# Optimization experiments

Measured on AMD Instinct MI355X. Metric: run time of the kernel, lower is better.

## Reference

```python
import jax, jax.numpy as jnp
import numpy as np

N_FLUID, N_BOX, K_MAX, KS, NCELL = 6000, 3000, 80, 4, 64
RADIUS = np.float32(0.5 * 1.5 * 6 * 0.025)  # filter_extent / 2 = 0.1125


def _ball_to_cube(p):
    """Volume-preserving ball->cube mapping (open3d ContinuousConv convention).
    p: [..., 3] coordinates in the unit ball; returns coords in [-1,1]^3."""
    eps = 1e-12
    x, y, z = p[..., 0], p[..., 1], p[..., 2]
    sq = x * x + y * y + z * z
    norm = jnp.sqrt(sq)
    rxy2 = x * x + y * y
    # sphere -> cylinder (volume preserving)
    polar = 1.25 * z * z > rxy2
    s_pol = jnp.sqrt(3.0 * norm / (norm + jnp.abs(z) + eps))
    s_eq = norm / jnp.sqrt(rxy2 + eps)
    xc = jnp.where(polar, s_pol * x, s_eq * x)
    yc = jnp.where(polar, s_pol * y, s_eq * y)
    zc = jnp.where(polar, jnp.sign(z) * norm, 1.5 * z * s_eq)
    zero = sq < 1e-12
    xc = jnp.where(zero, 0.0, xc)
    yc = jnp.where(zero, 0.0, yc)
    zc = jnp.where(zero, 0.0, zc)
    # cylinder -> cube (area-preserving disc -> square on xy)
    rxy = jnp.sqrt(xc * xc + yc * yc)
    FP = 4.0 / np.pi
    safe_x = jnp.where(jnp.abs(xc) < eps, eps, xc)
    safe_y = jnp.where(jnp.abs(yc) < eps, eps, yc)
    cond = jnp.abs(xc) >= jnp.abs(yc)
    u1 = jnp.sign(xc) * rxy
    v1 = u1 * FP * jnp.arctan(yc / safe_x)
    v2 = jnp.sign(yc) * rxy
    u2 = v2 * FP * jnp.arctan(xc / safe_y)
    u = jnp.where(cond, u1, u2)
    v = jnp.where(cond, v1, v2)
    small = rxy < eps
    u = jnp.where(small, 0.0, u)
    v = jnp.where(small, 0.0, v)
    return jnp.stack([u, v, zc], axis=-1)


def build_neighbors(pos_in, pos_out, ignore_self):
    """Fixed-radius neighbor search (capped at K_MAX) + window + trilinear
    interpolation cells/weights. Returns idx [No,K], cells [No,K,8] int32,
    coef [No,K,8] (trilinear weight * poly6 window * validity)."""
    d = pos_in[None, :, :] - pos_out[:, None, :]            # [No,Ni,3]
    d2 = jnp.sum(d * d, axis=-1)
    if ignore_self:
        ii = jnp.arange(pos_out.shape[0])
        d2 = jnp.where(ii[:, None] == ii[None, :], jnp.inf, d2)
    neg = jnp.where(d2 <= RADIUS * RADIUS, -d2, -jnp.inf)
    vals, idx = jax.lax.top_k(neg, K_MAX)                   # [No,K]
    valid = (vals > -jnp.inf).astype(pos_in.dtype)
    rel = (pos_in[idx] - pos_out[:, None, :]) / RADIUS      # [No,K,3] unit ball
    r2 = jnp.sum(rel * rel, axis=-1)
    win = jnp.clip((1.0 - r2) ** 3, 0.0, 1.0) * valid       # poly6 window
    g = jnp.clip((_ball_to_cube(rel) + 1.0) * 0.5 * (KS - 1), 0.0, KS - 1.0)
    i0 = jnp.clip(jnp.floor(g), 0, KS - 2).astype(jnp.int32)
    t = g - i0.astype(g.dtype)
    cells, tw = [], []
    for dx in (0, 1):
        for dy in (0, 1):
            for dz in (0, 1):
                w = ((t[..., 0] if dx else 1.0 - t[..., 0])
                     * (t[..., 1] if dy else 1.0 - t[..., 1])
                     * (t[..., 2] if dz else 1.0 - t[..., 2]))
                cell = ((i0[..., 2] + dz) * KS + (i0[..., 1] + dy)) * KS + (i0[..., 0] + dx)
                cells.append(cell)
                tw.append(w)
    cells = jnp.stack(cells, axis=-1)                       # [No,K,8]
    coef = jnp.stack(tw, axis=-1) * win[..., None]          # [No,K,8]
    return idx, cells, coef


def apply_cconv(feats_in, idx, cells, coef, W, b):
    """Continuous conv: scatter neighbor feats into 64 kernel cells per query,
    then contract with the filter. W: [64, F, O]."""
    N, K = idx.shape
    F = feats_in.shape[-1]
    nf = feats_in[idx]                                      # [N,K,F]
    S = jnp.zeros((N * NCELL, F), feats_in.dtype)
    row = (jnp.arange(N, dtype=jnp.int32) * NCELL)[:, None]
    for c in range(8):                                      # 8 trilinear corners
        flat = (row + cells[..., c]).reshape(-1)
        S = S.at[flat].add((coef[..., c:c + 1] * nf).reshape(-1, F))
    return jnp.einsum('ncf,cfo->no', S.reshape(N, NCELL, F), W) + b


def setup_inputs() -> dict:
    key = jax.random.key(0)
    ks = jax.random.split(key, 16)

    def p(i, shape, scale=0.05):
        return (scale * jax.random.normal(ks[i], shape)).astype(jnp.float32)

    return {
        'pos': jax.random.uniform(ks[0], (N_FLUID, 3), dtype=jnp.float32),
        'vel': jax.random.normal(ks[1], (N_FLUID, 3), dtype=jnp.float32),
        'box': jax.random.uniform(ks[2], (N_BOX, 3), dtype=jnp.float32),
        'box_feats': jax.random.normal(ks[3], (N_BOX, 3), dtype=jnp.float32),
        'cf_w': p(4, (NCELL, 4, 32)), 'cf_b': jnp.zeros((32,), jnp.float32),
        'co_w': p(5, (NCELL, 3, 32)), 'co_b': jnp.zeros((32,), jnp.float32),
        'd0_w': p(6, (4, 32)), 'd0_b': jnp.zeros((32,), jnp.float32),
        'c1_w': p(7, (NCELL, 96, 64)), 'c1_b': jnp.zeros((64,), jnp.float32),
        'd1_w': p(8, (96, 64)), 'd1_b': jnp.zeros((64,), jnp.float32),
        'c2_w': p(9, (NCELL, 64, 64)), 'c2_b': jnp.zeros((64,), jnp.float32),
        'd2_w': p(10, (64, 64)), 'd2_b': jnp.zeros((64,), jnp.float32),
        'c3_w': p(11, (NCELL, 64, 3)), 'c3_b': jnp.zeros((3,), jnp.float32),
        'd3_w': p(12, (64, 3)), 'd3_b': jnp.zeros((3,), jnp.float32),
    }


def reference(pos, vel, box, box_feats, cf_w, cf_b, co_w, co_b, d0_w, d0_b,
              c1_w, c1_b, d1_w, d1_b, c2_w, c2_b, d2_w, d2_b, c3_w, c3_b,
              d3_w, d3_b):
    fidx, fcells, fcoef = build_neighbors(pos, pos, True)
    oidx, ocells, ocoef = build_neighbors(box, pos, False)
    ff = jnp.concatenate([jnp.ones_like(pos[:, :1]), vel], axis=-1)  # [N,4]
    a_cf = apply_cconv(ff, fidx, fcells, fcoef, cf_w, cf_b)
    a_co = apply_cconv(box_feats, oidx, ocells, ocoef, co_w, co_b)
    a_d0 = ff @ d0_w + d0_b
    x = jnp.concatenate([a_co, a_cf, a_d0], axis=-1)                 # [N,96]
    for cw, cb, dw, db in ((c1_w, c1_b, d1_w, d1_b),
                           (c2_w, c2_b, d2_w, d2_b),
                           (c3_w, c3_b, d3_w, d3_b)):
        h = jax.nn.relu(x)
        y = apply_cconv(h, fidx, fcells, fcoef, cw, cb) + (h @ dw + db)
        x = y + x if y.shape[-1] == x.shape[-1] else y
    return x * (1.0 / 128.0)  # pos_correction [N,3]
```

## Files before the change

kernel.cpp:

```cpp
#include <hip/hip_runtime.h>
#include <math.h>

namespace {

constexpr int NQ  = 6000;
constexpr int NB  = 3000;
constexpr int K   = 80;
constexpr float RAD = 0.1125f;
constexpr float R2  = RAD * RAD;
constexpr float EPSF = 1e-12f;

constexpr int GS  = 8;
constexpr int NC  = GS*GS*GS;
constexpr int NO  = 65 * 64;
constexpr int NBLK = (NQ + 3) / 4;
constexpr int NBLK8 = ((NBLK + 7) / 8) * 8;

typedef __attribute__((ext_vector_type(8))) short bf16x8;
typedef __attribute__((ext_vector_type(4))) float f32x4;

__device__ __forceinline__ float sgn(float x) {
    return (x > 0.f) ? 1.f : ((x < 0.f) ? -1.f : 0.f);
}

__device__ __forceinline__ unsigned int bf16rne(float f) {
    unsigned int u = __float_as_uint(f);
    return (u + 0x7fffu + ((u >> 16) & 1u)) >> 16;
}
__device__ __forceinline__ float bf16f(unsigned short u) {
    return __uint_as_float(((unsigned int)u) << 16);
}
__device__ __forceinline__ int cell_of(float x, float y, float z) {
    int cx = min(max((int)(x * (float)GS), 0), GS-1);
    int cy = min(max((int)(y * (float)GS), 0), GS-1);
    int cz = min(max((int)(z * (float)GS), 0), GS-1);
    return (cz*GS + cy)*GS + cx;
}

__device__ void coef_store(float ddx, float ddy, float ddz, int slot,
                           int* __restrict__ cells, float* __restrict__ coefs)
{
    float rx = ddx / RAD, ry = ddy / RAD, rz = ddz / RAD;
    float r2 = rx*rx + ry*ry + rz*rz;
    float w1 = 1.f - r2;
    float win = (w1 > 0.f) ? w1*w1*w1 : 0.f;
    float norm = sqrtf(r2);
    float rxy2 = rx*rx + ry*ry;
    float xc, yc, zc;
    if (r2 < 1e-12f) {
        xc = yc = zc = 0.f;
    } else if (1.25f * rz * rz > rxy2) {
        float s = sqrtf(3.0f * norm / (norm + fabsf(rz) + EPSF));
        xc = s * rx; yc = s * ry; zc = sgn(rz) * norm;
    } else {
        float s = norm / sqrtf(rxy2 + EPSF);
        xc = s * rx; yc = s * ry; zc = 1.5f * rz * s;
    }
    float rxy = sqrtf(xc*xc + yc*yc);
    const float FP = (float)(4.0 / M_PI);
    float u, v;
    if (rxy < EPSF) {
        u = 0.f; v = 0.f;
    } else if (fabsf(xc) >= fabsf(yc)) {
        float sx = (fabsf(xc) < EPSF) ? EPSF : xc;
        u = sgn(xc) * rxy;
        v = u * FP * atanf(yc / sx);
    } else {
        float sy = (fabsf(yc) < EPSF) ? EPSF : yc;
        v = sgn(yc) * rxy;
        u = v * FP * atanf(xc / sy);
    }
    float gx = fminf(fmaxf((u  + 1.f) * 0.5f * 3.f, 0.f), 3.f);
    float gy = fminf(fmaxf((v  + 1.f) * 0.5f * 3.f, 0.f), 3.f);
    float gz = fminf(fmaxf((zc + 1.f) * 0.5f * 3.f, 0.f), 3.f);
    int ix = min((int)floorf(gx), 2);
    int iy = min((int)floorf(gy), 2);
    int iz = min((int)floorf(gz), 2);
    float tx = gx - (float)ix, ty = gy - (float)iy, tz = gz - (float)iz;
    cells[slot] = iz*16 + iy*4 + ix;
    float wx[2] = {1.f - tx, tx}, wy[2] = {1.f - ty, ty}, wz[2] = {1.f - tz, tz};
    float* cf = coefs + (size_t)slot * 8;
#pragma unroll
    for (int c = 0; c < 8; ++c)
        cf[c] = wx[c >> 2] * wy[(c >> 1) & 1] * wz[c & 1] * win;
}

__global__ __launch_bounds__(512) void scan_kernel(
    const int* __restrict__ gcnt,
    int* __restrict__ gs_f, int* __restrict__ gs_b,
    int* __restrict__ cur_f, int* __restrict__ cur_b)
{
    __shared__ int tmp[NC];
    int tid = threadIdx.x;
#pragma unroll
    for (int a = 0; a < 2; ++a) {
        int cntv = gcnt[a*NC + tid];
        tmp[tid] = cntv;
        __syncthreads();
        for (int off = 1; off < NC; off <<= 1) {
            int v = (tid >= off) ? tmp[tid - off] : 0;
            __syncthreads();
            tmp[tid] += v;
            __syncthreads();
        }
        int* gsd = a ? gs_b : gs_f;
        int* cur = a ? cur_b : cur_f;
        int excl = tmp[tid] - cntv;
        gsd[tid] = excl;
        cur[tid] = excl;
        if (tid == NC - 1) gsd[NC] = tmp[tid];
        __syncthreads();
    }
}

__global__ __launch_bounds__(256) void scatter_pts_kernel(
    const float* __restrict__ pos, const float* __restrict__ box,
    int* __restrict__ cur_f, int* __restrict__ cur_b,
    float* __restrict__ spf, int* __restrict__ sif,
    float* __restrict__ spb, int* __restrict__ sib)
{
    int t = blockIdx.x * blockDim.x + threadIdx.x;
    if (t < NQ) {
        float x = pos[t*3], y = pos[t*3+1], z = pos[t*3+2];
        int dst = atomicAdd(&cur_f[cell_of(x,y,z)], 1);
        spf[dst*3] = x; spf[dst*3+1] = y; spf[dst*3+2] = z;
        sif[dst] = t;
    } else if (t < NQ + NB) {
        int b = t - NQ;
        float x = box[b*3], y = box[b*3+1], z = box[b*3+2];
        int dst = atomicAdd(&cur_b[cell_of(x,y,z)], 1);
        spb[dst*3] = x; spb[dst*3+1] = y; spb[dst*3+2] = z;
        sib[dst] = b;
    }
}

__global__ __launch_bounds__(256) void nn2gc_kernel(
    const float* __restrict__ pos,
    const float* __restrict__ spf, const int* __restrict__ sif, const int* __restrict__ gsf,
    const float* __restrict__ spb, const int* __restrict__ sib, const int* __restrict__ gsb,
    int* __restrict__ f_cnt, int* __restrict__ f_idx, float* __restrict__ f_d2,
    int* __restrict__ f_cell, float* __restrict__ f_coef,
    int* __restrict__ b_cnt, int* __restrict__ b_idx, float* __restrict__ b_d2,
    int* __restrict__ b_cell, float* __restrict__ b_coef)
{
    int gw = (blockIdx.x * blockDim.x + threadIdx.x) >> 6;
    int lane = threadIdx.x & 63;
    if (gw >= 2 * NQ) return;
    bool isF = gw < NQ;
    int wid = isF ? gw : gw - NQ;
    const float* sp = isF ? spf : spb;
    const int*   si = isF ? sif : sib;
    const int*   gs = isF ? gsf : gsb;
    int*   cnt   = isF ? f_cnt  : b_cnt;
    int*   idxs  = isF ? f_idx  : b_idx;
    float* d2s   = isF ? f_d2   : b_d2;
    int*   cells = isF ? f_cell : b_cell;
    float* coefs = isF ? f_coef : b_coef;
    float qx = pos[wid*3+0], qy = pos[wid*3+1], qz = pos[wid*3+2];
    int cx = min(max((int)(qx * (float)GS), 0), GS-1);
    int cy = min(max((int)(qy * (float)GS), 0), GS-1);
    int cz = min(max((int)(qz * (float)GS), 0), GS-1);
    int x0 = max(cx-1, 0), x1 = min(cx+1, GS-1);
    int base = wid * K;
    int c = 0;
    for (int dz = -1; dz <= 1; ++dz) {
        int z = cz + dz; if ((unsigned)z >= (unsigned)GS) continue;
        for (int dy = -1; dy <= 1; ++dy) {
            int y = cy + dy; if ((unsigned)y >= (unsigned)GS) continue;
            int row = (z*GS + y)*GS;
            int s0 = gs[row + x0], s1 = gs[row + x1 + 1];
            for (int j0 = s0; j0 < s1; j0 += 64) {
                int ii = j0 + lane;
                float d2 = 1e30f; int oj = 0;
                float ddx = 0.f, ddy = 0.f, ddz = 0.f;
                if (ii < s1) {
                    oj = si[ii];
                    ddx = sp[ii*3+0]-qx; ddy = sp[ii*3+1]-qy; ddz = sp[ii*3+2]-qz;
                    d2 = ddx*ddx + ddy*ddy + ddz*ddz;
                    if (isF && oj == wid) d2 = 1e30f;
                }
                bool hit = d2 <= R2;
                unsigned long long m = __ballot(hit);
                int pc = __popcll(m);
                if (pc == 0) continue;
                if (c + pc <= K) {
                    if (hit) {
                        int p = c + __popcll(m & ((1ull << lane) - 1ull));
                        idxs[base + p] = oj;
                        d2s [base + p] = d2;
                        coef_store(ddx, ddy, ddz, base + p, cells, coefs);
                    }
                    c += pc;
                } else {
                    while (m) {
                        int l = __ffsll((unsigned long long)m) - 1;
                        m &= m - 1ull;
                        float dd = __shfl(d2, l);
                        int jv = __shfl(oj, l);
                        float ax = __shfl(ddx, l), ay = __shfl(ddy, l), az = __shfl(ddz, l);
                        int slot = -1;
                        if (c < K) { slot = c; c++; }
                        else {
                            float mx = -1.f; int am = 0;
                            for (int s = 0; s < K; ++s) {
                                float v = d2s[base + s];
                                if (v > mx) { mx = v; am = s; }
                            }
                            if (dd < mx) slot = am;
                        }
                        if (slot >= 0 && lane == 0) {
                            idxs[base + slot] = jv;
                            d2s [base + slot] = dd;
                            coef_store(ax, ay, az, base + slot, cells, coefs);
                        }
                    }
                }
            }
        }
    }
    if (lane == 0) cnt[wid] = c;
}

__global__ __launch_bounds__(256) void gather0_kernel(
    const int* __restrict__ order,
    const int* __restrict__ f_cnt, const int* __restrict__ f_idx,
    const int* __restrict__ f_cell, const float* __restrict__ f_coef,
    const int* __restrict__ b_cnt, const int* __restrict__ b_idx,
    const int* __restrict__ b_cell, const float* __restrict__ b_coef,
    const unsigned short* __restrict__ G0f, const unsigned short* __restrict__ G0b,
    const float* __restrict__ cfb, const float* __restrict__ cob,
    float* __restrict__ x1)
{
    __shared__ __align__(16) float coefF[K * 8];
    __shared__ __align__(16) float coefB[K * 8];
    __shared__ int jF[K], cF[K], jB[K], cBx[K];
    __shared__ float partF[8][32], partB[8][32];
    int lb = (blockIdx.x & 7) * (gridDim.x >> 3) + (blockIdx.x >> 3);
    int tid = threadIdx.x;
    int wv = tid >> 6, lane = tid & 63;
    int h = lane >> 5, o = lane & 31;
    int r = wv * 2 + h;
    int n = order[lb];
    int cnf = f_cnt[n], cnb = b_cnt[n];
    {
        const float4* srcF = (const float4*)(f_coef + (size_t)n * K * 8);
        const float4* srcB = (const float4*)(b_coef + (size_t)n * K * 8);
        for (int i = tid; i < cnf * 2; i += 256) ((float4*)coefF)[i] = srcF[i];
        for (int i = tid; i < cnb * 2; i += 256) ((float4*)coefB)[i] = srcB[i];
        for (int i = tid; i < cnf; i += 256) { jF[i] = f_idx[n*K + i]; cF[i]  = f_cell[n*K + i]; }
        for (int i = tid; i < cnb; i += 256) { jB[i] = b_idx[n*K + i]; cBx[i] = b_cell[n*K + i]; }
    }
    __syncthreads();
    float af = 0.f;
#pragma unroll 2
    for (int k = r; k < cnf; k += 8) {
        const unsigned short* Gj = G0f + (size_t)jF[k] * 2048 + (size_t)cF[k] * 32 + o;
        float4 cA = *reinterpret_cast<const float4*>(coefF + k*8);
        float4 cB = *reinterpret_cast<const float4*>(coefF + k*8 + 4);
        af += cA.x * bf16f(Gj[ 0 * 32]);
        af += cA.y * bf16f(Gj[16 * 32]);
        af += cA.z * bf16f(Gj[ 4 * 32]);
        af += cA.w * bf16f(Gj[20 * 32]);
        af += cB.x * bf16f(Gj[ 1 * 32]);
        af += cB.y * bf16f(Gj[17 * 32]);
        af += cB.z * bf16f(Gj[ 5 * 32]);
        af += cB.w * bf16f(Gj[21 * 32]);
    }
    float ab = 0.f;
#pragma unroll 2
    for (int k = r; k < cnb; k += 8) {
        const unsigned short* Gj = G0b + (size_t)jB[k] * 2048 + (size_t)cBx[k] * 32 + o;
        float4 cA = *reinterpret_cast<const float4*>(coefB + k*8);
        float4 cB = *reinterpret_cast<const float4*>(coefB + k*8 + 4);
        ab += cA.x * bf16f(Gj[ 0 * 32]);
        ab += cA.y * bf16f(Gj[16 * 32]);
        ab += cA.z * bf16f(Gj[ 4 * 32]);
        ab += cA.w * bf16f(Gj[20 * 32]);
        ab += cB.x * bf16f(Gj[ 1 * 32]);
        ab += cB.y * bf16f(Gj[17 * 32]);
        ab += cB.z * bf16f(Gj[ 5 * 32]);
        ab += cB.w * bf16f(Gj[21 * 32]);
    }
    partF[r][o] = af;
    partB[r][o] = ab;
    __syncthreads();
    if (tid < 64) {
        int oo = tid & 31;
        if (tid < 32) {
            float s = cfb[oo];
#pragma unroll
            for (int q = 0; q < 8; ++q) s += partF[q][oo];
            x1[(size_t)n * 96 + 32 + oo] = s;
        } else {
            float s = cob[oo];
#pragma unroll
            for (int q = 0; q < 8; ++q) s += partB[q][oo];
            x1[(size_t)n * 96 + oo] = s;
        }
    }
}

template<int F>
__global__ __launch_bounds__(256) void gemmGm_kernel(
    const float* __restrict__ feats,
    const unsigned short* __restrict__ Bt,
    unsigned short* __restrict__ G,
    int M)
{
    constexpr int NT = 5;
    constexpr int AST = F + 8;
    __shared__ unsigned short As[64 * AST];
    __shared__ unsigned short Bs[64 * AST];
    int tid = threadIdx.x, lane = tid & 63, wv = tid >> 6;
    int m0 = blockIdx.x * 64;
    int nt0 = blockIdx.y * NT;
    for (int i = tid; i < 64 * F / 4; i += 256) {
        int m = i / (F / 4), k4 = i % (F / 4);
        int gm = m0 + m; if (gm >= M) gm = M - 1;
        float4 av = *reinterpret_cast<const float4*>(feats + (size_t)gm * F + k4 * 4);
        uint2 ov;
        ov.x = bf16rne(fmaxf(av.x, 0.f)) | (bf16rne(fmaxf(av.y, 0.f)) << 16);
        ov.y = bf16rne(fmaxf(av.z, 0.f)) | (bf16rne(fmaxf(av.w, 0.f)) << 16);
        *reinterpret_cast<uint2*>(As + m * AST + k4 * 4) = ov;
    }
    int mr = lane & 15, quad = lane >> 4;
    for (int t = 0; t < NT; ++t) {
        int no0 = (nt0 + t) * 64;
        __syncthreads();
        for (int i = tid; i < 64 * F / 8; i += 256) {
            int nn = i / (F / 8), k8 = i % (F / 8);
            *reinterpret_cast<uint4*>(Bs + nn * AST + k8 * 8) =
                *reinterpret_cast<const uint4*>(Bt + (size_t)(no0 + nn) * F + k8 * 8);
        }
        __syncthreads();
        f32x4 acc[4] = {{0.f,0.f,0.f,0.f},{0.f,0.f,0.f,0.f},
                        {0.f,0.f,0.f,0.f},{0.f,0.f,0.f,0.f}};
#pragma unroll
        for (int kc = 0; kc < F; kc += 32) {
            bf16x8 a = *reinterpret_cast<const bf16x8*>(As + (wv*16 + mr) * AST + kc + quad*8);
#pragma unroll
            for (int q = 0; q < 4; ++q) {
                bf16x8 b = *reinterpret_cast<const bf16x8*>(Bs + (q*16 + mr) * AST + kc + quad*8);
                acc[q] = __builtin_amdgcn_mfma_f32_16x16x32_bf16(a, b, acc[q], 0, 0, 0);
            }
        }
#pragma unroll
        for (int q = 0; q < 4; ++q) {
#pragma unroll
            for (int rr = 0; rr < 4; ++rr) {
                int gm = m0 + wv*16 + quad*4 + rr;
                if (gm < M)
                    G[(size_t)gm * NO + no0 + q*16 + mr] = (unsigned short)bf16rne(acc[q][rr]);
            }
        }
    }
}

template<int FUSEY>
__global__ __launch_bounds__(256) void gatherG_kernel(
    const int* __restrict__ order,
    const int* __restrict__ cnt, const int* __restrict__ nidx,
    const int* __restrict__ ncell, const float* __restrict__ ncoef,
    const unsigned short* __restrict__ G,
    const float* __restrict__ cb, const float* __restrict__ db,
    const float* __restrict__ resid, float* __restrict__ out,
    const float* __restrict__ W3p, float* __restrict__ Y)
{
    __shared__ __align__(16) float coefL[K * 8];
    __shared__ int jL[K];
    __shared__ int cbL[K];
    __shared__ float part[3][64];
    __shared__ float xs[64];
    int lb = (blockIdx.x & 7) * (gridDim.x >> 3) + (blockIdx.x >> 3);
    int tid = threadIdx.x;
    int wv = tid >> 6, lane = tid & 63;
    int n = order[lb];
    int cn = cnt[n];
    {
        const float4* src = (const float4*)(ncoef + (size_t)n * K * 8);
        float4* dst = (float4*)coefL;
        for (int i = tid; i < cn * 2; i += 256) dst[i] = src[i];
        for (int i = tid; i < cn; i += 256) {
            jL[i]  = nidx [n*K + i];
            cbL[i] = ncell[n*K + i];
        }
    }
    __syncthreads();
    float a0 = 0.f, a1 = 0.f, a2 = 0.f, a3 = 0.f;
#pragma unroll 2
    for (int k = wv; k < cn; k += 4) {
        int j    = jL[k];
        int cbse = cbL[k];
        float4 cA = *reinterpret_cast<const float4*>(coefL + k*8);
        float4 cB = *reinterpret_cast<const float4*>(coefL + k*8 + 4);
        const unsigned short* Gj = G + (size_t)j * NO + (size_t)cbse * 64 + lane;
        a0 += cA.x * bf16f(Gj[ 0 * 64]);
        a1 += cA.y * bf16f(Gj[16 * 64]);
        a2 += cA.z * bf16f(Gj[ 4 * 64]);
        a3 += cA.w * bf16f(Gj[20 * 64]);
        a0 += cB.x * bf16f(Gj[ 1 * 64]);
        a1 += cB.y * bf16f(Gj[17 * 64]);
        a2 += cB.z * bf16f(Gj[ 5 * 64]);
        a3 += cB.w * bf16f(Gj[21 * 64]);
    }
    float s = (a0 + a1) + (a2 + a3);
    if (wv > 0) part[wv - 1][lane] = s;
    __syncthreads();
    if (wv == 0) {
        float acc = cb[lane] + db[lane] + s
                  + part[0][lane] + part[1][lane] + part[2][lane];
        acc += bf16f(G[(size_t)n * NO + 64*64 + lane]);
        if (resid) acc += resid[(size_t)n * 64 + lane];
        if (!FUSEY) {
            out[(size_t)n * 64 + lane] = acc;
        } else {
            xs[lane] = fmaxf(acc, 0.f);
        }
    }
    if (FUSEY) {
        __syncthreads();
        for (int t = tid; t < 195; t += 256) {
            float sum = 0.f;
#pragma unroll 16
            for (int f = 0; f < 64; ++f) sum += xs[f] * W3p[f*195 + t];
            Y[(size_t)n * 195 + t] = sum;
        }
    }
}

__global__ __launch_bounds__(256) void prep_kernel(
    const float* __restrict__ c1w, const float* __restrict__ d1w,
    const float* __restrict__ c2w, const float* __restrict__ d2w,
    const float* __restrict__ c3w, const float* __restrict__ d3w,
    const float* __restrict__ pos, const float* __restrict__ box,
    const float* __restrict__ vel, const float* __restrict__ bfeat,
    const float* __restrict__ cfw, const float* __restrict__ cow,
    const float* __restrict__ d0w, const float* __restrict__ d0b,
    unsigned short* __restrict__ Bt1, unsigned short* __restrict__ Bt2,
    unsigned short* __restrict__ G0f, unsigned short* __restrict__ G0b,
    float* __restrict__ W3p, float* __restrict__ x1,
    int* __restrict__ gcnt)
{
    int stride = gridDim.x * blockDim.x;
    int gid = blockIdx.x * blockDim.x + threadIdx.x;
    for (int i = gid; i < NQ + NB; i += stride) {
        const float* p = (i < NQ) ? pos + (size_t)i*3 : box + (size_t)(i-NQ)*3;
        atomicAdd(&gcnt[((i < NQ) ? 0 : NC) + cell_of(p[0], p[1], p[2])], 1);
    }
    for (int i = gid; i < NQ * 1024; i += stride) {
        int j = i >> 10, rr = i & 1023, c = rr >> 4, op = (rr & 15) * 2;
        float vx = vel[j*3+0], vy = vel[j*3+1], vz = vel[j*3+2];
        const float* w = cfw + (size_t)c * 128;
        float s0 = w[op]   + vx*w[32+op]   + vy*w[64+op]   + vz*w[96+op];
        float s1 = w[op+1] + vx*w[32+op+1] + vy*w[64+op+1] + vz*w[96+op+1];
        *reinterpret_cast<unsigned int*>(G0f + (size_t)j * 2048 + c*32 + op) =
            bf16rne(s0) | (bf16rne(s1) << 16);
    }
    for (int i = gid; i < NB * 1024; i += stride) {
        int j = i >> 10, rr = i & 1023, c = rr >> 4, op = (rr & 15) * 2;
        float b0 = bfeat[j*3+0], b1 = bfeat[j*3+1], b2 = bfeat[j*3+2];
        const float* w = cow + (size_t)c * 96;
        float s0 = b0*w[op]   + b1*w[32+op]   + b2*w[64+op];
        float s1 = b0*w[op+1] + b1*w[32+op+1] + b2*w[64+op+1];
        *reinterpret_cast<unsigned int*>(G0b + (size_t)j * 2048 + c*32 + op) =
            bf16rne(s0) | (bf16rne(s1) << 16);
    }
    for (int i = gid; i < NO * 96; i += stride) {
        int n = i / 96, f = i % 96, c = n >> 6, o = n & 63;
        float v = (c < 64) ? c1w[((size_t)c*96 + f)*64 + o] : d1w[f*64 + o];
        Bt1[i] = (unsigned short)bf16rne(v);
    }
    for (int i = gid; i < NO * 64; i += stride) {
        int n = i / 64, f = i % 64, c = n >> 6, o = n & 63;
        float v = (c < 64) ? c2w[((size_t)c*64 + f)*64 + o] : d2w[f*64 + o];
        Bt2[i] = (unsigned short)bf16rne(v);
    }
    for (int i = gid; i < 64 * 195; i += stride) {
        int f = i / 195, r = i % 195, c = r / 3, o = r % 3;
        W3p[i] = (c < 64) ? c3w[(c*64 + f)*3 + o] : d3w[f*3 + o];
    }
    for (int i = gid; i < NQ * 32; i += stride) {
        int n = i >> 5, o = i & 31;
        float acc = d0b[o] + d0w[o]
                  + vel[n*3+0] * d0w[32 + o]
                  + vel[n*3+1] * d0w[64 + o]
                  + vel[n*3+2] * d0w[96 + o];
        x1[n*96 + 64 + o] = acc;
    }
}

__global__ __launch_bounds__(256) void gather3_kernel(
    const int* __restrict__ order,
    const int* __restrict__ cnt, const int* __restrict__ nidx,
    const int* __restrict__ ncell, const float* __restrict__ ncoef,
    const float* __restrict__ Y,
    const float* __restrict__ cb3, const float* __restrict__ db3,
    float* __restrict__ out)
{
    int lb = (blockIdx.x & 7) * (gridDim.x >> 3) + (blockIdx.x >> 3);
    int gw = lb * 4 + ((int)threadIdx.x >> 6);
    int lane = threadIdx.x & 63;
    if (gw >= NQ) return;
    int n = order[gw];
    int cn = cnt[n];
    float a0 = 0.f, a1 = 0.f, a2 = 0.f;
#pragma unroll
    for (int seg = 0; seg < 2; ++seg) {
        int kidx = seg * 64 + lane;
        if (kidx < cn) {
            int j  = nidx [n*K + kidx];
            int cb = ncell[n*K + kidx];
            const float* cf = ncoef + (size_t)(n*K + kidx) * 8;
            const float* Yj = Y + (size_t)j * 195;
#pragma unroll
            for (int c = 0; c < 8; ++c) {
                int cell = cb + (c & 1)*16 + ((c >> 1) & 1)*4 + (c >> 2);
                float wgt = cf[c];
                const float* Tp = Yj + cell*3;
                a0 += wgt * Tp[0];
                a1 += wgt * Tp[1];
                a2 += wgt * Tp[2];
            }
        }
    }
#pragma unroll
    for (int s = 32; s > 0; s >>= 1) {
        a0 += __shfl_down(a0, s);
        a1 += __shfl_down(a1, s);
        a2 += __shfl_down(a2, s);
    }
    if (lane == 0) {
        const float* Yn = Y + (size_t)n * 195 + 192;
        out[n*3+0] = (a0 + Yn[0] + cb3[0] + db3[0]) * (1.f/128.f);
        out[n*3+1] = (a1 + Yn[1] + cb3[1] + db3[1]) * (1.f/128.f);
        out[n*3+2] = (a2 + Yn[2] + cb3[2] + db3[2]) * (1.f/128.f);
    }
}

}

extern "C" void kernel_launch(void* const* d_in, const int* in_sizes, int n_in,
                              void* d_out, int out_size, void* d_ws, size_t ws_size,
                              hipStream_t stream)
{
    const float* pos       = (const float*)d_in[0];
    const float* vel       = (const float*)d_in[1];
    const float* box       = (const float*)d_in[2];
    const float* box_feats = (const float*)d_in[3];
    const float* cf_w = (const float*)d_in[4];  const float* cf_b = (const float*)d_in[5];
    const float* co_w = (const float*)d_in[6];  const float* co_b = (const float*)d_in[7];
    const float* d0_w = (const float*)d_in[8];  const float* d0_b = (const float*)d_in[9];
    const float* c1_w = (const float*)d_in[10]; const float* c1_b = (const float*)d_in[11];
    const float* d1_w = (const float*)d_in[12]; const float* d1_b = (const float*)d_in[13];
    const float* c2_w = (const float*)d_in[14]; const float* c2_b = (const float*)d_in[15];
    const float* d2_w = (const float*)d_in[16]; const float* d2_b = (const float*)d_in[17];
    const float* c3_w = (const float*)d_in[18]; const float* c3_b = (const float*)d_in[19];
    const float* d3_w = (const float*)d_in[20]; const float* d3_b = (const float*)d_in[21];

    char* wsb = (char*)d_ws;
    size_t off = 0;
    auto alloc = [&](size_t bytes) {
        void* p = wsb + off;
        off = (off + bytes + 255) & ~(size_t)255;
        return p;
    };
    char*  Graw = (char*)alloc((size_t)NQ * NO * 2 + 4096);
    unsigned short* G = (unsigned short*)Graw;
    float* f_d2 = (float*)Graw;
    float* b_d2 = (float*)Graw + (size_t)NQ * K;
    unsigned short* G0f = (unsigned short*)(Graw + ((size_t)4 << 20));
    unsigned short* G0b = (unsigned short*)(Graw + ((size_t)32 << 20));
    int*   f_cnt  = (int*)  alloc((size_t)NQ * 4);
    int*   f_idx  = (int*)  alloc((size_t)NQ * K * 4);
    int*   f_cell = (int*)  alloc((size_t)NQ * K * 4);
    float* f_coef = (float*)alloc((size_t)NQ * K * 8 * 4);
    int*   b_cnt  = (int*)  alloc((size_t)NQ * 4);
    int*   b_idx  = (int*)  alloc((size_t)NQ * K * 4);
    int*   b_cell = (int*)  alloc((size_t)NQ * K * 4);
    float* b_coef = (float*)alloc((size_t)NQ * K * 8 * 4);
    float* x1     = (float*)alloc((size_t)NQ * 96 * 4);
    float* x2     = (float*)alloc((size_t)NQ * 64 * 4);
    unsigned short* Bt1 = (unsigned short*)alloc((size_t)NO * 96 * 2);
    unsigned short* Bt2 = (unsigned short*)alloc((size_t)NO * 64 * 2);
    float* W3p    = (float*)alloc((size_t)64 * 195 * 4);
    float* Y      = (float*)alloc((size_t)NQ * 195 * 4);
    int*   gcnt   = (int*)  alloc((size_t)2 * NC * 4);
    int*   gs_f   = (int*)  alloc((size_t)(NC + 1) * 4);
    int*   gs_b   = (int*)  alloc((size_t)(NC + 1) * 4);
    int*   cur_f  = (int*)  alloc((size_t)NC * 4);
    int*   cur_b  = (int*)  alloc((size_t)NC * 4);
    float* spf    = (float*)alloc((size_t)NQ * 3 * 4);
    int*   sif    = (int*)  alloc((size_t)NQ * 4);
    float* spb    = (float*)alloc((size_t)NB * 3 * 4);
    int*   sib    = (int*)  alloc((size_t)NB * 4);

    dim3 b256(256);
    hipMemsetAsync(gcnt, 0, (size_t)2 * NC * 4, stream);
    prep_kernel<<<512, b256, 0, stream>>>(c1_w, d1_w, c2_w, d2_w, c3_w, d3_w,
                                          pos, box, vel, box_feats, cf_w, co_w,
                                          d0_w, d0_b,
                                          Bt1, Bt2, G0f, G0b, W3p, x1, gcnt);
    scan_kernel<<<1, 512, 0, stream>>>(gcnt, gs_f, gs_b, cur_f, cur_b);
    scatter_pts_kernel<<<(NQ + NB + 255)/256, b256, 0, stream>>>(
        pos, box, cur_f, cur_b, spf, sif, spb, sib);
    nn2gc_kernel<<<(2*NQ*64 + 255)/256, b256, 0, stream>>>(
        pos, spf, sif, gs_f, spb, sib, gs_b,
        f_cnt, f_idx, f_d2, f_cell, f_coef,
        b_cnt, b_idx, b_d2, b_cell, b_coef);
    gather0_kernel<<<NQ, b256, 0, stream>>>(sif,
        f_cnt, f_idx, f_cell, f_coef,
        b_cnt, b_idx, b_cell, b_coef,
        G0f, G0b, cf_b, co_b, x1);
    gemmGm_kernel<96><<<dim3((NQ+63)/64, 13), b256, 0, stream>>>(x1, Bt1, G, NQ);
    gatherG_kernel<0><<<NQ, b256, 0, stream>>>(sif, f_cnt, f_idx, f_cell, f_coef,
        G, c1_b, d1_b, nullptr, x2, nullptr, nullptr);
    gemmGm_kernel<64><<<dim3((NQ+63)/64, 13), b256, 0, stream>>>(x2, Bt2, G, NQ);
    gatherG_kernel<1><<<NQ, b256, 0, stream>>>(sif, f_cnt, f_idx, f_cell, f_coef,
        G, c2_b, d2_b, x2, nullptr, W3p, Y);
    gather3_kernel<<<NBLK8, b256, 0, stream>>>(sif, f_cnt, f_idx, f_cell, f_coef,
        Y, c3_b, d3_b, (float*)d_out);

    (void)in_sizes; (void)n_in; (void)out_size; (void)ws_size;
    (void)f_d2; (void)b_d2;
}
```

Baseline: 270.0 us.

## Merge grid histogram into scan kernel and co-schedule weight prep with neighbor search

Cell counting moves into a single 1024-thread block that builds histograms in shared memory and scans both grids at once, which removes the memset and one launch. The weight/G0 precompute work moves into the first 512 blocks of the neighbor-search kernel so it runs alongside the search rather than as a separate serial launch. The gather kernels also precompute combined neighbor*cell offsets in shared memory, saving an LDS array and some address arithmetic. The risk is that the prep blocks and search blocks compete for CUs, and that the single-block histogram serializes on shared-memory atomics.

```diff
diff --git a/kernel.cpp b/kernel.cpp
--- a/kernel.cpp
+++ b/kernel.cpp
@@ -15,6 +15,7 @@
 constexpr int NO  = 65 * 64;
 constexpr int NBLK = (NQ + 3) / 4;
 constexpr int NBLK8 = ((NBLK + 7) / 8) * 8;
+constexpr int PREPB = 512;
 
 typedef __attribute__((ext_vector_type(8))) short bf16x8;
 typedef __attribute__((ext_vector_type(4))) float f32x4;
@@ -85,32 +86,43 @@
         cf[c] = wx[c >> 2] * wy[(c >> 1) & 1] * wz[c & 1] * win;
 }
 
-__global__ __launch_bounds__(512) void scan_kernel(
-    const int* __restrict__ gcnt,
+__global__ __launch_bounds__(1024) void grid_build_kernel(
+    const float* __restrict__ pos, const float* __restrict__ box,
     int* __restrict__ gs_f, int* __restrict__ gs_b,
     int* __restrict__ cur_f, int* __restrict__ cur_b)
 {
-    __shared__ int tmp[NC];
+    __shared__ int cntF[NC], cntB[NC];
+    __shared__ int tmpF[NC], tmpB[NC];
     int tid = threadIdx.x;
-#pragma unroll
-    for (int a = 0; a < 2; ++a) {
-        int cntv = gcnt[a*NC + tid];
-        tmp[tid] = cntv;
+    int half = tid >> 9, t = tid & 511;
+    if (half == 0) cntF[t] = 0; else cntB[t] = 0;
+    __syncthreads();
+    for (int i = tid; i < NQ + NB; i += 1024) {
+        if (i < NQ) {
+            atomicAdd(&cntF[cell_of(pos[i*3], pos[i*3+1], pos[i*3+2])], 1);
+        } else {
+            int b = i - NQ;
+            atomicAdd(&cntB[cell_of(box[b*3], box[b*3+1], box[b*3+2])], 1);
+        }
+    }
+    __syncthreads();
+    int* cnt = half ? cntB : cntF;
+    int* tmp = half ? tmpB : tmpF;
+    int cv = cnt[t];
+    tmp[t] = cv;
+    __syncthreads();
+    for (int off = 1; off < NC; off <<= 1) {
+        int v = (t >= off) ? tmp[t - off] : 0;
         __syncthreads();
-        for (int off = 1; off < NC; off <<= 1) {
-            int v = (tid >= off) ? tmp[tid - off] : 0;
-            __syncthreads();
-            tmp[tid] += v;
-            __syncthreads();
-        }
-        int* gsd = a ? gs_b : gs_f;
-        int* cur = a ? cur_b : cur_f;
-        int excl = tmp[tid] - cntv;
-        gsd[tid] = excl;
-        cur[tid] = excl;
-        if (tid == NC - 1) gsd[NC] = tmp[tid];
+        tmp[t] += v;
         __syncthreads();
     }
+    int* gsd = half ? gs_b : gs_f;
+    int* cur = half ? cur_b : cur_f;
+    int excl = tmp[t] - cv;
+    gsd[t] = excl;
+    cur[t] = excl;
+    if (t == NC - 1) gsd[NC] = tmp[t];
 }
 
 __global__ __launch_bounds__(256) void scatter_pts_kernel(
@@ -141,9 +153,63 @@
     int* __restrict__ f_cnt, int* __restrict__ f_idx, float* __restrict__ f_d2,
     int* __restrict__ f_cell, float* __restrict__ f_coef,
     int* __restrict__ b_cnt, int* __restrict__ b_idx, float* __restrict__ b_d2,
-    int* __restrict__ b_cell, float* __restrict__ b_coef)
-{
-    int gw = (blockIdx.x * blockDim.x + threadIdx.x) >> 6;
+    int* __restrict__ b_cell, float* __restrict__ b_coef,
+    const float* __restrict__ c1w, const float* __restrict__ d1w,
+    const float* __restrict__ c2w, const float* __restrict__ d2w,
+    const float* __restrict__ c3w, const float* __restrict__ d3w,
+    const float* __restrict__ vel, const float* __restrict__ bfeat,
+    const float* __restrict__ cfw, const float* __restrict__ cow,
+    const float* __restrict__ d0w, const float* __restrict__ d0b,
+    unsigned short* __restrict__ Bt1, unsigned short* __restrict__ Bt2,
+    unsigned short* __restrict__ G0f, unsigned short* __restrict__ G0b,
+    float* __restrict__ W3p, float* __restrict__ x1)
+{
+    if (blockIdx.x < PREPB) {
+        int stride = PREPB * 256;
+        int gid = blockIdx.x * 256 + threadIdx.x;
+        for (int i = gid; i < NQ * 1024; i += stride) {
+            int j = i >> 10, rr = i & 1023, c = rr >> 4, op = (rr & 15) * 2;
+            float vx = vel[j*3+0], vy = vel[j*3+1], vz = vel[j*3+2];
+            const float* w = cfw + (size_t)c * 128;
+            float s0 = w[op]   + vx*w[32+op]   + vy*w[64+op]   + vz*w[96+op];
+            float s1 = w[op+1] + vx*w[32+op+1] + vy*w[64+op+1] + vz*w[96+op+1];
+            *reinterpret_cast<unsigned int*>(G0f + (size_t)j * 2048 + c*32 + op) =
+                bf16rne(s0) | (bf16rne(s1) << 16);
+        }
+        for (int i = gid; i < NB * 1024; i += stride) {
+            int j = i >> 10, rr = i & 1023, c = rr >> 4, op = (rr & 15) * 2;
+            float b0 = bfeat[j*3+0], b1 = bfeat[j*3+1], b2 = bfeat[j*3+2];
+            const float* w = cow + (size_t)c * 96;
+            float s0 = b0*w[op]   + b1*w[32+op]   + b2*w[64+op];
+            float s1 = b0*w[op+1] + b1*w[32+op+1] + b2*w[64+op+1];
+            *reinterpret_cast<unsigned int*>(G0b + (size_t)j * 2048 + c*32 + op) =
+                bf16rne(s0) | (bf16rne(s1) << 16);
+        }
+        for (int i = gid; i < NO * 96; i += stride) {
+            int n = i / 96, f = i % 96, c = n >> 6, o = n & 63;
+            float v = (c < 64) ? c1w[((size_t)c*96 + f)*64 + o] : d1w[f*64 + o];
+            Bt1[i] = (unsigned short)bf16rne(v);
+        }
+        for (int i = gid; i < NO * 64; i += stride) {
+            int n = i / 64, f = i % 64, c = n >> 6, o = n & 63;
+            float v = (c < 64) ? c2w[((size_t)c*64 + f)*64 + o] : d2w[f*64 + o];
+            Bt2[i] = (unsigned short)bf16rne(v);
+        }
+        for (int i = gid; i < 64 * 195; i += stride) {
+            int f = i / 195, r = i % 195, c = r / 3, o = r % 3;
+            W3p[i] = (c < 64) ? c3w[(c*64 + f)*3 + o] : d3w[f*3 + o];
+        }
+        for (int i = gid; i < NQ * 32; i += stride) {
+            int n = i >> 5, o = i & 31;
+            float acc = d0b[o] + d0w[o]
+                      + vel[n*3+0] * d0w[32 + o]
+                      + vel[n*3+1] * d0w[64 + o]
+                      + vel[n*3+2] * d0w[96 + o];
+            x1[n*96 + 64 + o] = acc;
+        }
+        return;
+    }
+    int gw = (int)(blockIdx.x - PREPB) * 4 + ((int)threadIdx.x >> 6);
     int lane = threadIdx.x & 63;
     if (gw >= 2 * NQ) return;
     bool isF = gw < NQ;
@@ -160,7 +226,7 @@
     int cx = min(max((int)(qx * (float)GS), 0), GS-1);
     int cy = min(max((int)(qy * (float)GS), 0), GS-1);
     int cz = min(max((int)(qz * (float)GS), 0), GS-1);
-    int x0 = max(cx-1, 0), x1 = min(cx+1, GS-1);
+    int x0 = max(cx-1, 0), x1c = min(cx+1, GS-1);
     int base = wid * K;
     int c = 0;
     for (int dz = -1; dz <= 1; ++dz) {
@@ -168,7 +234,7 @@
         for (int dy = -1; dy <= 1; ++dy) {
             int y = cy + dy; if ((unsigned)y >= (unsigned)GS) continue;
             int row = (z*GS + y)*GS;
-            int s0 = gs[row + x0], s1 = gs[row + x1 + 1];
+            int s0 = gs[row + x0], s1 = gs[row + x1c + 1];
             for (int j0 = s0; j0 < s1; j0 += 64) {
                 int ii = j0 + lane;
                 float d2 = 1e30f; int oj = 0;
@@ -233,7 +299,7 @@
 {
     __shared__ __align__(16) float coefF[K * 8];
     __shared__ __align__(16) float coefB[K * 8];
-    __shared__ int jF[K], cF[K], jB[K], cBx[K];
+    __shared__ int jF[K], jB[K];
     __shared__ float partF[8][32], partB[8][32];
     int lb = (blockIdx.x & 7) * (gridDim.x >> 3) + (blockIdx.x >> 3);
     int tid = threadIdx.x;
@@ -247,14 +313,14 @@
         const float4* srcB = (const float4*)(b_coef + (size_t)n * K * 8);
         for (int i = tid; i < cnf * 2; i += 256) ((float4*)coefF)[i] = srcF[i];
         for (int i = tid; i < cnb * 2; i += 256) ((float4*)coefB)[i] = srcB[i];
-        for (int i = tid; i < cnf; i += 256) { jF[i] = f_idx[n*K + i]; cF[i]  = f_cell[n*K + i]; }
-        for (int i = tid; i < cnb; i += 256) { jB[i] = b_idx[n*K + i]; cBx[i] = b_cell[n*K + i]; }
+        for (int i = tid; i < cnf; i += 256) jF[i] = f_idx[n*K + i] * 2048 + f_cell[n*K + i] * 32;
+        for (int i = tid; i < cnb; i += 256) jB[i] = b_idx[n*K + i] * 2048 + b_cell[n*K + i] * 32;
     }
     __syncthreads();
     float af = 0.f;
 #pragma unroll 2
     for (int k = r; k < cnf; k += 8) {
-        const unsigned short* Gj = G0f + (size_t)jF[k] * 2048 + (size_t)cF[k] * 32 + o;
+        const unsigned short* Gj = G0f + jF[k] + o;
         float4 cA = *reinterpret_cast<const float4*>(coefF + k*8);
         float4 cB = *reinterpret_cast<const float4*>(coefF + k*8 + 4);
         af += cA.x * bf16f(Gj[ 0 * 32]);
@@ -269,7 +335,7 @@
     float ab = 0.f;
 #pragma unroll 2
     for (int k = r; k < cnb; k += 8) {
-        const unsigned short* Gj = G0b + (size_t)jB[k] * 2048 + (size_t)cBx[k] * 32 + o;
+        const unsigned short* Gj = G0b + jB[k] + o;
         float4 cA = *reinterpret_cast<const float4*>(coefB + k*8);
         float4 cB = *reinterpret_cast<const float4*>(coefB + k*8 + 4);
         ab += cA.x * bf16f(Gj[ 0 * 32]);
@@ -368,7 +434,6 @@
 {
     __shared__ __align__(16) float coefL[K * 8];
     __shared__ int jL[K];
-    __shared__ int cbL[K];
     __shared__ float part[3][64];
     __shared__ float xs[64];
     int lb = (blockIdx.x & 7) * (gridDim.x >> 3) + (blockIdx.x >> 3);
@@ -380,20 +445,16 @@
         const float4* src = (const float4*)(ncoef + (size_t)n * K * 8);
         float4* dst = (float4*)coefL;
         for (int i = tid; i < cn * 2; i += 256) dst[i] = src[i];
-        for (int i = tid; i < cn; i += 256) {
-            jL[i]  = nidx [n*K + i];
-            cbL[i] = ncell[n*K + i];
-        }
+        for (int i = tid; i < cn; i += 256)
+            jL[i] = nidx[n*K + i] * NO + ncell[n*K + i] * 64;
     }
     __syncthreads();
     float a0 = 0.f, a1 = 0.f, a2 = 0.f, a3 = 0.f;
 #pragma unroll 2
     for (int k = wv; k < cn; k += 4) {
-        int j    = jL[k];
-        int cbse = cbL[k];
         float4 cA = *reinterpret_cast<const float4*>(coefL + k*8);
         float4 cB = *reinterpret_cast<const float4*>(coefL + k*8 + 4);
-        const unsigned short* Gj = G + (size_t)j * NO + (size_t)cbse * 64 + lane;
+        const unsigned short* Gj = G + jL[k] + lane;
         a0 += cA.x * bf16f(Gj[ 0 * 64]);
         a1 += cA.y * bf16f(Gj[16 * 64]);
         a2 += cA.z * bf16f(Gj[ 4 * 64]);
@@ -425,67 +486,6 @@
             for (int f = 0; f < 64; ++f) sum += xs[f] * W3p[f*195 + t];
             Y[(size_t)n * 195 + t] = sum;
         }
-    }
-}
-
-__global__ __launch_bounds__(256) void prep_kernel(
-    const float* __restrict__ c1w, const float* __restrict__ d1w,
-    const float* __restrict__ c2w, const float* __restrict__ d2w,
-    const float* __restrict__ c3w, const float* __restrict__ d3w,
-    const float* __restrict__ pos, const float* __restrict__ box,
-    const float* __restrict__ vel, const float* __restrict__ bfeat,
-    const float* __restrict__ cfw, const float* __restrict__ cow,
-    const float* __restrict__ d0w, const float* __restrict__ d0b,
-    unsigned short* __restrict__ Bt1, unsigned short* __restrict__ Bt2,
-    unsigned short* __restrict__ G0f, unsigned short* __restrict__ G0b,
-    float* __restrict__ W3p, float* __restrict__ x1,
-    int* __restrict__ gcnt)
-{
-    int stride = gridDim.x * blockDim.x;
-    int gid = blockIdx.x * blockDim.x + threadIdx.x;
-    for (int i = gid; i < NQ + NB; i += stride) {
-        const float* p = (i < NQ) ? pos + (size_t)i*3 : box + (size_t)(i-NQ)*3;
-        atomicAdd(&gcnt[((i < NQ) ? 0 : NC) + cell_of(p[0], p[1], p[2])], 1);
-    }
-    for (int i = gid; i < NQ * 1024; i += stride) {
-        int j = i >> 10, rr = i & 1023, c = rr >> 4, op = (rr & 15) * 2;
-        float vx = vel[j*3+0], vy = vel[j*3+1], vz = vel[j*3+2];
-        const float* w = cfw + (size_t)c * 128;
-        float s0 = w[op]   + vx*w[32+op]   + vy*w[64+op]   + vz*w[96+op];
-        float s1 = w[op+1] + vx*w[32+op+1] + vy*w[64+op+1] + vz*w[96+op+1];
-        *reinterpret_cast<unsigned int*>(G0f + (size_t)j * 2048 + c*32 + op) =
-            bf16rne(s0) | (bf16rne(s1) << 16);
-    }
-    for (int i = gid; i < NB * 1024; i += stride) {
-        int j = i >> 10, rr = i & 1023, c = rr >> 4, op = (rr & 15) * 2;
-        float b0 = bfeat[j*3+0], b1 = bfeat[j*3+1], b2 = bfeat[j*3+2];
-        const float* w = cow + (size_t)c * 96;
-        float s0 = b0*w[op]   + b1*w[32+op]   + b2*w[64+op];
-        float s1 = b0*w[op+1] + b1*w[32+op+1] + b2*w[64+op+1];
-        *reinterpret_cast<unsigned int*>(G0b + (size_t)j * 2048 + c*32 + op) =
-            bf16rne(s0) | (bf16rne(s1) << 16);
-    }
-    for (int i = gid; i < NO * 96; i += stride) {
-        int n = i / 96, f = i % 96, c = n >> 6, o = n & 63;
-        float v = (c < 64) ? c1w[((size_t)c*96 + f)*64 + o] : d1w[f*64 + o];
-        Bt1[i] = (unsigned short)bf16rne(v);
-    }
-    for (int i = gid; i < NO * 64; i += stride) {
-        int n = i / 64, f = i % 64, c = n >> 6, o = n & 63;
-        float v = (c < 64) ? c2w[((size_t)c*64 + f)*64 + o] : d2w[f*64 + o];
-        Bt2[i] = (unsigned short)bf16rne(v);
-    }
-    for (int i = gid; i < 64 * 195; i += stride) {
-        int f = i / 195, r = i % 195, c = r / 3, o = r % 3;
-        W3p[i] = (c < 64) ? c3w[(c*64 + f)*3 + o] : d3w[f*3 + o];
-    }
-    for (int i = gid; i < NQ * 32; i += stride) {
-        int n = i >> 5, o = i & 31;
-        float acc = d0b[o] + d0w[o]
-                  + vel[n*3+0] * d0w[32 + o]
-                  + vel[n*3+1] * d0w[64 + o]
-                  + vel[n*3+2] * d0w[96 + o];
-        x1[n*96 + 64 + o] = acc;
     }
 }
 
@@ -584,7 +584,6 @@
     unsigned short* Bt2 = (unsigned short*)alloc((size_t)NO * 64 * 2);
     float* W3p    = (float*)alloc((size_t)64 * 195 * 4);
     float* Y      = (float*)alloc((size_t)NQ * 195 * 4);
-    int*   gcnt   = (int*)  alloc((size_t)2 * NC * 4);
     int*   gs_f   = (int*)  alloc((size_t)(NC + 1) * 4);
     int*   gs_b   = (int*)  alloc((size_t)(NC + 1) * 4);
     int*   cur_f  = (int*)  alloc((size_t)NC * 4);
@@ -595,18 +594,16 @@
     int*   sib    = (int*)  alloc((size_t)NB * 4);
 
     dim3 b256(256);
-    hipMemsetAsync(gcnt, 0, (size_t)2 * NC * 4, stream);
-    prep_kernel<<<512, b256, 0, stream>>>(c1_w, d1_w, c2_w, d2_w, c3_w, d3_w,
-                                          pos, box, vel, box_feats, cf_w, co_w,
-                                          d0_w, d0_b,
-                                          Bt1, Bt2, G0f, G0b, W3p, x1, gcnt);
-    scan_kernel<<<1, 512, 0, stream>>>(gcnt, gs_f, gs_b, cur_f, cur_b);
+    grid_build_kernel<<<1, 1024, 0, stream>>>(pos, box, gs_f, gs_b, cur_f, cur_b);
     scatter_pts_kernel<<<(NQ + NB + 255)/256, b256, 0, stream>>>(
         pos, box, cur_f, cur_b, spf, sif, spb, sib);
-    nn2gc_kernel<<<(2*NQ*64 + 255)/256, b256, 0, stream>>>(
+    nn2gc_kernel<<<PREPB + (2*NQ + 3)/4, b256, 0, stream>>>(
         pos, spf, sif, gs_f, spb, sib, gs_b,
         f_cnt, f_idx, f_d2, f_cell, f_coef,
-        b_cnt, b_idx, b_d2, b_cell, b_coef);
+        b_cnt, b_idx, b_d2, b_cell, b_coef,
+        c1_w, d1_w, c2_w, d2_w, c3_w, d3_w,
+        vel, box_feats, cf_w, co_w, d0_w, d0_b,
+        Bt1, Bt2, G0f, G0b, W3p, x1);
     gather0_kernel<<<NQ, b256, 0, stream>>>(sif,
         f_cnt, f_idx, f_cell, f_coef,
         b_cnt, b_idx, b_cell, b_coef,
```

Result: faster. 255.2 us (-5.5%).
